# Kernel optimization log

Hardware: AMD Instinct MI355X
Metric: run time of the kernel (lower is better)

## Reference

```python
import jax, jax.numpy as jnp
import numpy as np

B, R, L, D, V, P = 128, 30, 60, 300, 50000, 3

def setup_inputs() -> dict:
    key = jax.random.key(0)
    ks = jax.random.split(key, 24)
    u = lambda k, shp: jax.random.uniform(k, shp, jnp.float32, -0.1, 0.1)
    inp = {
        'user_reviews': jax.random.randint(ks[0], (B, R, L), 0, V),
        'item_reviews': jax.random.randint(ks[1], (B, R, L), 0, V),
        'user_emb': u(ks[2], (V, D)),
        'item_emb': u(ks[3], (V, D)),
        'g1_w': u(ks[4], (D, D)), 'g1_b': u(ks[5], (D,)),
        'g2_w': u(ks[6], (D, D)), 'g2_b': u(ks[7], (D,)),
        # per-pointer review-level co-attention params (gumbel=True, pooling=max)
        'Mr': jax.random.normal(ks[8], (P, D, D)),
        'Wur': jax.random.normal(ks[9], (P, D, D)) * 0.05, 'bur': jnp.zeros((P, D)),
        'Wir': jax.random.normal(ks[10], (P, D, D)) * 0.05, 'bir': jnp.zeros((P, D)),
        # per-pointer word-level co-attention params (gumbel=False, pooling=avg)
        'Mw': jax.random.normal(ks[11], (P, D, D)),
        'Wuw': jax.random.normal(ks[12], (P, D, D)) * 0.05, 'buw': jnp.zeros((P, D)),
        'Wiw': jax.random.normal(ks[13], (P, D, D)) * 0.05, 'biw': jnp.zeros((P, D)),
        # FM params, pred_in_dim = 2*P*D (pointer_agg='concat')
        'fm_w0': jnp.zeros((1,)),
        'fm_w': jnp.zeros((2 * P * D,)),
        'fm_v': jax.random.normal(ks[14], (2 * P * D, 10)) * 0.01,
    }
    return inp

def _review_gate(embs, g1_w, g1_b, g2_w, g2_b):
    # embs: [B,R,L,D] -> [B,R,D]
    s = embs.sum(2)
    return jax.nn.sigmoid(s @ g1_w.T + g1_b) * jnp.tanh(s @ g2_w.T + g2_b)

def _coatt_scores(u_fea, i_fea, Wu, bu, Wi, bi, M):
    u = u_fea @ Wu.T + bu
    i = i_fea @ Wi.T + bi
    return jnp.einsum('brd,de,bse->brs', u, M, i)  # [B,R,R] or [B,L,L]

def reference(user_reviews, item_reviews, user_emb, item_emb,
              g1_w, g1_b, g2_w, g2_b,
              Mr, Wur, bur, Wir, bir,
              Mw, Wuw, buw, Wiw, biw,
              fm_w0, fm_w, fm_v):
    gkey = jax.random.key(42)
    u_embs = user_emb[user_reviews]  # [B,R,L,D]
    i_embs = item_emb[item_reviews]
    u_rev = _review_gate(u_embs, g1_w, g1_b, g2_w, g2_b)  # [B,R,D]
    i_rev = _review_gate(i_embs, g1_w, g1_b, g2_w, g2_b)
    u_reps, i_reps = [], []
    for p in range(P):
        # review-level co-attention, max pooling, gumbel hard (top-1 pointer)
        s = _coatt_scores(u_rev, i_rev, Wur[p], bur[p], Wir[p], bir[p], Mr[p])
        u_score = s.max(2)   # [B,R]
        i_score = s.max(1)   # [B,R]
        gu = jax.random.gumbel(jax.random.fold_in(gkey, 2 * p), u_score.shape)
        gi = jax.random.gumbel(jax.random.fold_in(gkey, 2 * p + 1), i_score.shape)
        # hard one-hot bmm gather + .long() re-embed == argmax review select
        # (the .long() cast in torch severs the straight-through grad path)
        idx_u = jnp.argmax(u_score + gu, axis=1)  # [B]
        idx_i = jnp.argmax(i_score + gi, axis=1)
        u_tok = jnp.take_along_axis(user_reviews, idx_u[:, None, None], axis=1)[:, 0]  # [B,L]
        i_tok = jnp.take_along_axis(item_reviews, idx_i[:, None, None], axis=1)[:, 0]
        u_words = user_emb[u_tok]  # [B,L,D]
        i_words = item_emb[i_tok]
        # word-level co-attention, avg pooling, soft attention
        s2 = _coatt_scores(u_words, i_words, Wuw[p], buw[p], Wiw[p], biw[p], Mw[p])
        p_u = jax.nn.softmax(s2.mean(2), axis=1)  # [B,L]
        p_i = jax.nn.softmax(s2.mean(1), axis=1)
        u_reps.append(jnp.einsum('bld,bl->bd', u_words, p_u))
        i_reps.append(jnp.einsum('bld,bl->bd', i_words, p_i))
    u_fea = jnp.concatenate(u_reps, axis=1)  # [B, P*D] (pointer_agg='concat')
    i_fea = jnp.concatenate(i_reps, axis=1)
    joint = jnp.concatenate([u_fea, i_fea], axis=1)  # [B, 2*P*D]; dropout is identity (eval)
    # Factorization Machine
    linear = fm_w0 + jnp.sum(fm_w * joint, axis=1, keepdims=True)
    inter = 0.5 * jnp.sum((joint @ fm_v) ** 2 - (joint ** 2) @ (fm_v ** 2), axis=1, keepdims=True)
    return (linear + inter)[:, 0]  # [B]
```

## Files before the change

kernel.cpp:

```cpp
#include <hip/hip_runtime.h>
#include <stdint.h>
#include <math.h>


__host__ __device__ static inline void tf2x32(uint32_t k0, uint32_t k1,
                                              uint32_t x0, uint32_t x1,
                                              uint32_t* o0, uint32_t* o1) {
  uint32_t ks[3] = {k0, k1, k0 ^ k1 ^ 0x1BD11BDAu};
  x0 += ks[0]; x1 += ks[1];
  const int rotA[4] = {13, 15, 26, 6};
  const int rotB[4] = {17, 29, 16, 24};
#pragma unroll
  for (int i = 0; i < 5; ++i) {
    const int* rot = ((i & 1) == 0) ? rotA : rotB;
#pragma unroll
    for (int j = 0; j < 4; ++j) {
      x0 += x1;
      x1 = (x1 << rot[j]) | (x1 >> (32 - rot[j]));
      x1 ^= x0;
    }
    x0 += ks[(i + 1) % 3];
    x1 += ks[(i + 2) % 3] + (uint32_t)(i + 1);
  }
  *o0 = x0; *o1 = x1;
}

struct GKeys { uint32_t v[12]; };
struct Ptr6 {
  const float* X[6];
  const float* W[6];
  const float* Bb[6];
  float*       Y[6];
};

__device__ static inline float jax_gumbel32(uint32_t k0, uint32_t k1, uint32_t idx) {
  uint32_t o0, o1;
  tf2x32(k0, k1, 0u, idx, &o0, &o1);
  uint32_t bits = o0 ^ o1;
  float f = __uint_as_float((bits >> 9) | 0x3f800000u) - 1.0f;
  float u = (f > 0.0f) ? f : 1.17549435e-38f;
  return -logf(-logf(u));
}

#define MODE_NN 0
#define MODE_NT 1
#define MODE_TN 2

template <int MODE, bool BIAS>
__device__ __forceinline__ void gemm_tile(float* __restrict__ sm,
                                          const float* __restrict__ X,
                                          const float* __restrict__ W,
                                          const float* __restrict__ bias,
                                          float* __restrict__ Y,
                                          float* __restrict__ Yt,
                                          int M, int bm, int n0, int t) {
  float (*Xs)[68] = (float(*)[68])sm;
  float (*Ws_)[68] = (float(*)[68])(sm + 20 * 68);
  const bool act = t < 256;
  int tm4 = ((t >> 4) & 15) * 4;
  int tn4 = (t & 15) * 4;
  float acc[4][4] = {{0.f}};
  int xm = t >> 2;
  int xk = (t & 3) * 5;
  for (int k0 = 0; k0 < 300; k0 += 20) {
    if (act) {
      if (MODE == MODE_TN) {
#pragma unroll
        for (int i = 0; i < 5; ++i) {
          int flat = t + i * 256;
          int kk = flat >> 6, nn = flat & 63;
          int r = bm + nn;
          Xs[kk][nn] = (r < 300) ? X[(size_t)(k0 + kk) * 300 + r] : 0.f;
        }
      } else {
        int rr = bm + xm; if (rr >= M) rr = M - 1;
        const float* xp = X + (size_t)rr * 300 + k0 + xk;
#pragma unroll
        for (int j = 0; j < 5; ++j) Xs[xk + j][xm] = xp[j];
      }
      if (MODE == MODE_NT) {
        int d = n0 + xm;
        bool ok = d < 300;
        const float* wp = W + (size_t)d * 300 + k0 + xk;
#pragma unroll
        for (int j = 0; j < 5; ++j) Ws_[xk + j][xm] = ok ? wp[j] : 0.f;
      } else {
#pragma unroll
        for (int i = 0; i < 5; ++i) {
          int flat = t + i * 256;
          int kk = flat >> 6, nn = flat & 63;
          int col = n0 + nn;
          Ws_[kk][nn] = (col < 300) ? W[(size_t)(k0 + kk) * 300 + col] : 0.f;
        }
      }
    }
    __syncthreads();
    if (act) {
#pragma unroll
      for (int kk = 0; kk < 20; ++kk) {
        const float4 a = *(const float4*)&Xs[kk][tm4];
        const float4 w = *(const float4*)&Ws_[kk][tn4];
        float av[4] = {a.x, a.y, a.z, a.w};
        float wv[4] = {w.x, w.y, w.z, w.w};
#pragma unroll
        for (int i = 0; i < 4; ++i)
#pragma unroll
          for (int j = 0; j < 4; ++j)
            acc[i][j] = fmaf(av[i], wv[j], acc[i][j]);
      }
    }
    __syncthreads();
  }
  if (!act) return;
  float bv[4] = {0.f, 0.f, 0.f, 0.f};
  if (BIAS) {
#pragma unroll
    for (int j = 0; j < 4; ++j) {
      int col = n0 + tn4 + j;
      if (col < 300) bv[j] = bias[col];
    }
  }
#pragma unroll
  for (int i = 0; i < 4; ++i) {
    int row = bm + tm4 + i;
    if (row < M) {
      float* yp = Y + (size_t)row * 300 + n0 + tn4;
#pragma unroll
      for (int j = 0; j < 4; ++j) {
        int col = n0 + tn4 + j;
        if (col < 300) yp[j] = acc[i][j] + bv[j];
      }
    }
  }
  if (Yt) {
#pragma unroll
    for (int i = 0; i < 4; ++i) {
      int row = bm + tm4 + i;
      if (row < 300) {
#pragma unroll
        for (int j = 0; j < 4; ++j) {
          int col = n0 + tn4 + j;
          if (col < 300) Yt[(size_t)col * 300 + row] = acc[i][j];
        }
      }
    }
  }
}

__global__ __launch_bounds__(256)
void weights_kernel(const float* __restrict__ Wur, const float* __restrict__ Mr,
                    const float* __restrict__ Mw, const float* __restrict__ Wiw,
                    const float* __restrict__ Wuw,
                    const float* __restrict__ bur, const float* __restrict__ buw,
                    const float* __restrict__ biw,
                    float* __restrict__ Wp, float* __restrict__ A1,
                    float* __restrict__ CGH, float* __restrict__ Bp) {
  __shared__ __align__(16) float arena[2720];
  int bid = blockIdx.x, t = threadIdx.x;
  if (bid < 75) {
    int z = bid / 25, r = bid % 25;
    gemm_tile<MODE_TN, false>(arena, Wur + (size_t)z * 90000, Mr + (size_t)z * 90000,
                              nullptr, Wp + (size_t)z * 90000, nullptr,
                              300, (r / 5) * 64, (r % 5) * 64, t);
  } else if (bid < 150) {
    int zi = bid - 75, z = zi / 25, r = zi % 25;
    gemm_tile<MODE_NN, false>(arena, Mw + (size_t)z * 90000, Wiw + (size_t)z * 90000,
                              nullptr, A1 + (size_t)z * 90000, nullptr,
                              300, (r / 5) * 64, (r % 5) * 64, t);
  } else {
    int z = bid - 150;
    float* vb = arena;
    float* t1s = arena + 304;
    float* t2s = arena + 608;
    const float* Mwz = Mw + (size_t)z * 90000;
    const float* Wuwz = Wuw + (size_t)z * 90000;
    const float* Wiwz = Wiw + (size_t)z * 90000;
    const float* Mrz = Mr + (size_t)z * 90000;
    for (int k = t; k < 300; k += 256) vb[k] = biw[z * 300 + k];
    __syncthreads();
    for (int e = t; e < 300; e += 256) {
      float a = 0.f;
      for (int k = 0; k < 300; ++k) a = fmaf(Mwz[(size_t)e * 300 + k], vb[k], a);
      t1s[e] = a;
    }
    __syncthreads();
    for (int k = t; k < 300; k += 256) {
      float a = 0.f;
      for (int d = 0; d < 300; ++d) a = fmaf(Wuwz[(size_t)d * 300 + k], t1s[d], a);
      CGH[(size_t)(2 * z) * 300 + k] = a;
    }
    __syncthreads();
    for (int d = t; d < 300; d += 256) vb[d] = buw[z * 300 + d];
    __syncthreads();
    for (int e = t; e < 300; e += 256) {
      float a = 0.f;
      for (int d = 0; d < 300; ++d) a = fmaf(Mwz[(size_t)d * 300 + e], vb[d], a);
      t2s[e] = a;
    }
    __syncthreads();
    for (int k = t; k < 300; k += 256) {
      float a = 0.f;
      for (int e = 0; e < 300; ++e) a = fmaf(Wiwz[(size_t)e * 300 + k], t2s[e], a);
      CGH[(size_t)(2 * z + 1) * 300 + k] = a;
    }
    __syncthreads();
    for (int d = t; d < 300; d += 256) vb[d] = bur[z * 300 + d];
    __syncthreads();
    for (int e = t; e < 300; e += 256) {
      float a = 0.f;
      for (int d = 0; d < 300; ++d) a = fmaf(Mrz[(size_t)d * 300 + e], vb[d], a);
      Bp[z * 300 + e] = a;
    }
  }
}

__global__ __launch_bounds__(320)
void gather_kernel(const int* __restrict__ uRevs, const int* __restrict__ iRevs,
                   const float* __restrict__ uEmb, const float* __restrict__ iEmb,
                   float* __restrict__ S) {
  int bid = blockIdx.x;
  int t = threadIdx.x;
  __shared__ int toks[4][60];
  if (t < 240) {
    int rr = t / 60, l = t - rr * 60;
    int grow = bid * 4 + rr;
    int side = grow / 3840;
    int row = grow - side * 3840;
    const int* revs = side ? iRevs : uRevs;
    toks[rr][l] = revs[row * 60 + l];
  }
  __syncthreads();
  if (t < 300) {
    int sub = t / 75;
    int q4 = (t - sub * 75) * 4;
    int grow = bid * 4 + sub;
    int side = grow / 3840;
    const float* emb = side ? iEmb : uEmb;
    const int* tk = toks[sub];
    float ax = 0.f, ay = 0.f, az = 0.f, aw = 0.f;
#pragma unroll
    for (int l0 = 0; l0 < 60; l0 += 15) {
      float4 v[15];
#pragma unroll
      for (int qq = 0; qq < 15; ++qq)
        v[qq] = *(const float4*)&emb[(size_t)tk[l0 + qq] * 300 + q4];
#pragma unroll
      for (int qq = 0; qq < 15; ++qq) {
        ax += v[qq].x; ay += v[qq].y; az += v[qq].z; aw += v[qq].w;
      }
    }
    float4 r = {ax, ay, az, aw};
    *(float4*)&S[(size_t)grow * 300 + q4] = r;
  }
}

__global__ __launch_bounds__(256)
void gate_kernel(const float* __restrict__ S,
                 const float* __restrict__ g1w, const float* __restrict__ g1b,
                 const float* __restrict__ g2w, const float* __restrict__ g2b,
                 float* __restrict__ REV,
                 const float* __restrict__ Wuw, const float* __restrict__ A1,
                 float* __restrict__ KG, float* __restrict__ KGT) {
  __shared__ __align__(16) float arena[4080];
  int bid = blockIdx.x, t = threadIdx.x;
  if (bid < 600) {
    float (*Xs)[68] = (float(*)[68])arena;
    float (*Ws1)[68] = (float(*)[68])(arena + 1360);
    float (*Ws2)[68] = (float(*)[68])(arena + 2720);
    int bm = (bid / 5) * 64;
    int n0 = (bid % 5) * 64;
    int tm4 = (t >> 4) * 4;
    int tn4 = (t & 15) * 4;
    float acc1[4][4] = {{0.f}};
    float acc2[4][4] = {{0.f}};
    int xm = t >> 2;
    int xk = (t & 3) * 5;
    for (int k0 = 0; k0 < 300; k0 += 20) {
      const float* xp = S + (size_t)(bm + xm) * 300 + k0 + xk;
#pragma unroll
      for (int j = 0; j < 5; ++j) Xs[xk + j][xm] = xp[j];
      {
        int dIdx = n0 + xm;
        bool ok = dIdx < 300;
        const float* wp1 = g1w + (size_t)dIdx * 300 + k0 + xk;
        const float* wp2 = g2w + (size_t)dIdx * 300 + k0 + xk;
#pragma unroll
        for (int j = 0; j < 5; ++j) Ws1[xk + j][xm] = ok ? wp1[j] : 0.f;
#pragma unroll
        for (int j = 0; j < 5; ++j) Ws2[xk + j][xm] = ok ? wp2[j] : 0.f;
      }
      __syncthreads();
#pragma unroll
      for (int kk = 0; kk < 20; ++kk) {
        const float4 a = *(const float4*)&Xs[kk][tm4];
        const float4 w1 = *(const float4*)&Ws1[kk][tn4];
        const float4 w2 = *(const float4*)&Ws2[kk][tn4];
        float av[4] = {a.x, a.y, a.z, a.w};
        float w1v[4] = {w1.x, w1.y, w1.z, w1.w};
        float w2v[4] = {w2.x, w2.y, w2.z, w2.w};
#pragma unroll
        for (int i = 0; i < 4; ++i)
#pragma unroll
          for (int j = 0; j < 4; ++j) {
            acc1[i][j] = fmaf(av[i], w1v[j], acc1[i][j]);
            acc2[i][j] = fmaf(av[i], w2v[j], acc2[i][j]);
          }
      }
      __syncthreads();
    }
#pragma unroll
    for (int i = 0; i < 4; ++i) {
      int row = bm + tm4 + i;
      float* yp = REV + (size_t)row * 300 + n0 + tn4;
#pragma unroll
      for (int j = 0; j < 4; ++j) {
        int col = n0 + tn4 + j;
        if (col < 300) {
          float a = acc1[i][j] + g1b[col];
          float b = acc2[i][j] + g2b[col];
          yp[j] = (1.f / (1.f + expf(-a))) * tanhf(b);
        }
      }
    }
  } else {
    int zi = bid - 600, z = zi / 25, r = zi % 25;
    gemm_tile<MODE_TN, false>(arena, Wuw + (size_t)z * 90000, A1 + (size_t)z * 90000,
                              nullptr, KG + (size_t)z * 90000,
                              KGT + (size_t)z * 90000,
                              300, (r / 5) * 64, (r % 5) * 64, t);
  }
}

__global__ __launch_bounds__(256)
void rev128_kernel(Ptr6 P) {
  int z = blockIdx.z;
  const bool nt = z >= 3;
  const float* __restrict__ X = P.X[z];
  const float* __restrict__ W = P.W[z];
  const float* __restrict__ bias = P.Bb[z];
  float* __restrict__ Y = P.Y[z];
  __shared__ __align__(16) float Xs[20][136];
  __shared__ __align__(16) float Ws_[20][68];
  int t = threadIdx.x;
  int bm = blockIdx.x * 128, n0 = blockIdx.y * 64;
  int tm8 = (t >> 4) * 8, tn4 = (t & 15) * 4;
  float acc[8][4] = {{0.f}};
  int xm = t >> 1, xk = (t & 1) * 10;
  int wm = t >> 2, wk = (t & 3) * 5;
  for (int k0 = 0; k0 < 300; k0 += 20) {
    const float* xp = X + (size_t)(bm + xm) * 300 + k0 + xk;
#pragma unroll
    for (int j = 0; j < 10; ++j) Xs[xk + j][xm] = xp[j];
    if (nt) {
      int d = n0 + wm;
      bool ok = d < 300;
      const float* wp = W + (size_t)d * 300 + k0 + wk;
#pragma unroll
      for (int j = 0; j < 5; ++j) Ws_[wk + j][wm] = ok ? wp[j] : 0.f;
    } else {
#pragma unroll
      for (int i = 0; i < 5; ++i) {
        int flat = t + i * 256;
        int kk = flat >> 6, nn = flat & 63;
        int col = n0 + nn;
        Ws_[kk][nn] = (col < 300) ? W[(size_t)(k0 + kk) * 300 + col] : 0.f;
      }
    }
    __syncthreads();
#pragma unroll
    for (int kk = 0; kk < 20; ++kk) {
      const float4 a0 = *(const float4*)&Xs[kk][tm8];
      const float4 a1 = *(const float4*)&Xs[kk][tm8 + 4];
      const float4 w = *(const float4*)&Ws_[kk][tn4];
      float av[8] = {a0.x, a0.y, a0.z, a0.w, a1.x, a1.y, a1.z, a1.w};
      float wv[4] = {w.x, w.y, w.z, w.w};
#pragma unroll
      for (int i = 0; i < 8; ++i)
#pragma unroll
        for (int j = 0; j < 4; ++j)
          acc[i][j] = fmaf(av[i], wv[j], acc[i][j]);
    }
    __syncthreads();
  }
  float bv[4];
#pragma unroll
  for (int j = 0; j < 4; ++j) {
    int col = n0 + tn4 + j;
    bv[j] = (col < 300) ? bias[col] : 0.f;
  }
#pragma unroll
  for (int i = 0; i < 8; ++i) {
    float* yp = Y + (size_t)(bm + tm8 + i) * 300 + n0 + tn4;
#pragma unroll
    for (int j = 0; j < 4; ++j) {
      int col = n0 + tn4 + j;
      if (col < 300) yp[j] = acc[i][j] + bv[j];
    }
  }
}

__global__ __launch_bounds__(256)
void argmax_mean_kernel(const float* __restrict__ Tall, const float* __restrict__ Iall,
                        const int* __restrict__ uRevs, const int* __restrict__ iRevs,
                        const float* __restrict__ uEmb, const float* __restrict__ iEmb,
                        int* __restrict__ idxU, int* __restrict__ idxI,
                        float* __restrict__ MEAN, GKeys K) {
  int b = blockIdx.x, z = blockIdx.y, t = threadIdx.x;
  uint32_t ku0 = K.v[z * 4], ku1 = K.v[z * 4 + 1];
  uint32_t ki0 = K.v[z * 4 + 2], ki1 = K.v[z * 4 + 3];
  __shared__ __align__(16) float Is[30 * 304];
  __shared__ float Sc[900];
  __shared__ float us[30], vs[30];
  __shared__ int selU, selI;
  __shared__ int toksI_s[60], toksU_s[60];
  const float* Tb = Tall + (size_t)z * 1152000 + (size_t)b * 9000;
  const float* Ib = Iall + (size_t)z * 1152000 + (size_t)b * 9000;
  for (int fc = t; fc < 2250; fc += 256) {
    int r = fc / 75, q = fc - r * 75;
    *(float4*)&Is[r * 304 + q * 4] = *(const float4*)&Ib[r * 300 + q * 4];
  }
  __syncthreads();
  for (int id = t; id < 900; id += 256) {
    int r = id / 30, c = id - r * 30;
    const float* tr = Tb + r * 300;
    const float* ic = Is + c * 304;
    float acc = 0.f;
    for (int k = 0; k < 300; k += 4) {
      float4 a = *(const float4*)&tr[k];
      float4 w = *(const float4*)&ic[k];
      acc = fmaf(a.x, w.x, acc);
      acc = fmaf(a.y, w.y, acc);
      acc = fmaf(a.z, w.z, acc);
      acc = fmaf(a.w, w.w, acc);
    }
    Sc[id] = acc;
  }
  __syncthreads();
  if (t < 30) {
    float m = -3.4e38f;
    for (int c = 0; c < 30; ++c) m = fmaxf(m, Sc[t * 30 + c]);
    us[t] = m + jax_gumbel32(ku0, ku1, (uint32_t)(b * 30 + t));
  } else if (t >= 64 && t < 94) {
    int s = t - 64;
    float m = -3.4e38f;
    for (int r = 0; r < 30; ++r) m = fmaxf(m, Sc[r * 30 + s]);
    vs[s] = m + jax_gumbel32(ki0, ki1, (uint32_t)(b * 30 + s));
  }
  __syncthreads();
  if (t == 0) {
    int best = 0; float bvv = us[0];
    for (int r = 1; r < 30; ++r) { if (us[r] > bvv) { bvv = us[r]; best = r; } }
    idxU[z * 128 + b] = best; selU = best;
  } else if (t == 1) {
    int best = 0; float bvv = vs[0];
    for (int s = 1; s < 30; ++s) { if (vs[s] > bvv) { bvv = vs[s]; best = s; } }
    idxI[z * 128 + b] = best; selI = best;
  }
  __syncthreads();
  if (t < 60) toksI_s[t] = iRevs[(b * 30 + selI) * 60 + t];
  else if (t >= 64 && t < 124) toksU_s[t - 64] = uRevs[(b * 30 + selU) * 60 + (t - 64)];
  __syncthreads();
  for (int dd = t; dd < 600; dd += 256) {
    int side = dd / 300;
    int d = dd - side * 300;
    const int* tk = side ? toksU_s : toksI_s;
    const float* em = side ? uEmb : iEmb;
    float acc = 0.f;
#pragma unroll
    for (int l0 = 0; l0 < 60; l0 += 10) {
      float v[10];
#pragma unroll
      for (int q = 0; q < 10; ++q)
        v[q] = em[(size_t)tk[l0 + q] * 300 + d];
#pragma unroll
      for (int q = 0; q < 10; ++q) acc += v[q];
    }
    MEAN[((size_t)(2 * z + side) * 128 + b) * 300 + d] = acc * (1.f / 60.f);
  }
}

__global__ __launch_bounds__(256)
void word_rep_kernel(const int* __restrict__ uRevs, const int* __restrict__ iRevs,
                     const float* __restrict__ uEmb, const float* __restrict__ iEmb,
                     const int* __restrict__ idxU, const int* __restrict__ idxI,
                     const float* __restrict__ MEAN, const float* __restrict__ KG,
                     const float* __restrict__ KGT, const float* __restrict__ CGH,
                     float* __restrict__ JNT) {
  int b = blockIdx.x, side = blockIdx.y, p = blockIdx.z;
  int zz = 2 * p + side;
  const int* revs = side ? iRevs : uRevs;
  const float* emb = side ? iEmb : uEmb;
  int idx = side ? idxI[p * 128 + b] : idxU[p * 128 + b];
  const float* Kmat = (side ? KGT : KG) + (size_t)p * 90000;
  __shared__ int toks[60];
  __shared__ float ms[300];
  __shared__ float g_s[300];
  __shared__ float score[60];
  __shared__ float probs[64];
  int t = threadIdx.x;
  if (t < 60) toks[t] = revs[(b * 30 + idx) * 60 + t];
  const float* mrow = MEAN + ((size_t)zz * 128 + b) * 300;
  for (int d = t; d < 300; d += 256) ms[d] = mrow[d];
  __syncthreads();
  for (int k = t; k < 300; k += 256) {
    const float* kr = Kmat + (size_t)k * 300;
    float acc = 0.f;
    for (int e = 0; e < 300; e += 4) {
      float4 kv = *(const float4*)&kr[e];
      acc = fmaf(kv.x, ms[e], acc);
      acc = fmaf(kv.y, ms[e + 1], acc);
      acc = fmaf(kv.z, ms[e + 2], acc);
      acc = fmaf(kv.w, ms[e + 3], acc);
    }
    g_s[k] = acc + CGH[(size_t)zz * 300 + k];
  }
  __syncthreads();
  int w = t >> 6, j = t & 63;
  for (int i = 0; i < 15; ++i) {
    int l = w * 15 + i;
    const float* er = emb + (size_t)toks[l] * 300;
    float partial = 0.f;
#pragma unroll
    for (int c = 0; c < 5; ++c) {
      int k = j + c * 64;
      if (k < 300) partial = fmaf(er[k], g_s[k], partial);
    }
#pragma unroll
    for (int m = 32; m >= 1; m >>= 1) partial += __shfl_xor(partial, m);
    if (j == 0) score[l] = partial;
  }
  __syncthreads();
  if (w == 0) {
    float s = (j < 60) ? score[j] : -3.4e38f;
    float m = s;
#pragma unroll
    for (int mm = 32; mm >= 1; mm >>= 1) m = fmaxf(m, __shfl_xor(m, mm));
    float e = (j < 60) ? expf(s - m) : 0.f;
    float sum = e;
#pragma unroll
    for (int mm = 32; mm >= 1; mm >>= 1) sum += __shfl_xor(sum, mm);
    if (j < 60) probs[j] = e / sum;
  }
  __syncthreads();
  float* outp = JNT + (size_t)b * 1800 + side * 900 + p * 300;
  for (int d = t; d < 300; d += 256) {
    float acc = 0.f;
    for (int l0 = 0; l0 < 60; l0 += 6) {
      float e0 = emb[(size_t)toks[l0 + 0] * 300 + d];
      float e1 = emb[(size_t)toks[l0 + 1] * 300 + d];
      float e2 = emb[(size_t)toks[l0 + 2] * 300 + d];
      float e3 = emb[(size_t)toks[l0 + 3] * 300 + d];
      float e4 = emb[(size_t)toks[l0 + 4] * 300 + d];
      float e5 = emb[(size_t)toks[l0 + 5] * 300 + d];
      acc = fmaf(probs[l0 + 0], e0, acc);
      acc = fmaf(probs[l0 + 1], e1, acc);
      acc = fmaf(probs[l0 + 2], e2, acc);
      acc = fmaf(probs[l0 + 3], e3, acc);
      acc = fmaf(probs[l0 + 4], e4, acc);
      acc = fmaf(probs[l0 + 5], e5, acc);
    }
    outp[d] = acc;
  }
}

__global__ __launch_bounds__(64)
void fm_kernel(const float* __restrict__ JNT, const float* __restrict__ w0,
               const float* __restrict__ fw, const float* __restrict__ fv,
               float* __restrict__ out) {
  int b = blockIdx.x, lane = threadIdx.x;
  const float* x = JNT + (size_t)b * 1800;
  float lin = 0.f;
  float t1[10], t2[10];
#pragma unroll
  for (int k = 0; k < 10; ++k) { t1[k] = 0.f; t2[k] = 0.f; }
  for (int j = lane; j < 1800; j += 64) {
    float xv = x[j];
    lin = fmaf(fw[j], xv, lin);
    float xx = xv * xv;
#pragma unroll
    for (int k = 0; k < 10; ++k) {
      float v = fv[j * 10 + k];
      t1[k] = fmaf(xv, v, t1[k]);
      t2[k] = fmaf(xx, v * v, t2[k]);
    }
  }
#pragma unroll
  for (int m = 32; m >= 1; m >>= 1) {
    lin += __shfl_xor(lin, m);
#pragma unroll
    for (int k = 0; k < 10; ++k) {
      t1[k] += __shfl_xor(t1[k], m);
      t2[k] += __shfl_xor(t2[k], m);
    }
  }
  if (lane == 0) {
    float inter = 0.f;
#pragma unroll
    for (int k = 0; k < 10; ++k) inter += t1[k] * t1[k] - t2[k];
    out[b] = w0[0] + lin + 0.5f * inter;
  }
}

extern "C" void kernel_launch(void* const* d_in, const int* in_sizes, int n_in,
                              void* d_out, int out_size, void* d_ws, size_t ws_size,
                              hipStream_t stream) {
  (void)in_sizes; (void)n_in; (void)out_size;
  const int*   uRevs = (const int*)d_in[0];
  const int*   iRevs = (const int*)d_in[1];
  const float* uEmb  = (const float*)d_in[2];
  const float* iEmb  = (const float*)d_in[3];
  const float* g1w   = (const float*)d_in[4];
  const float* g1b   = (const float*)d_in[5];
  const float* g2w   = (const float*)d_in[6];
  const float* g2b   = (const float*)d_in[7];
  const float* Mr    = (const float*)d_in[8];
  const float* Wur   = (const float*)d_in[9];
  const float* bur   = (const float*)d_in[10];
  const float* Wir   = (const float*)d_in[11];
  const float* bir   = (const float*)d_in[12];
  const float* Mw    = (const float*)d_in[13];
  const float* Wuw   = (const float*)d_in[14];
  const float* buw   = (const float*)d_in[15];
  const float* Wiw   = (const float*)d_in[16];
  const float* biw   = (const float*)d_in[17];
  const float* fmw0  = (const float*)d_in[18];
  const float* fmw   = (const float*)d_in[19];
  const float* fmv   = (const float*)d_in[20];
  float* out = (float*)d_out;

  float* ws = (float*)d_ws;
  const size_t NEED_BYTES = (size_t)10298700 * 4;
  if (ws_size < NEED_BYTES) return;

  float* S     = ws + 0;
  float* TPall = ws + 0;
  float* REV   = ws + 3456000;
  float* MEAN  = ws + 3456000;
  float* JNT   = ws + 3916800;
  int*   idxU  = (int*)(ws + 4147200);
  int*   idxI  = idxU + 384;
  float* IPall = ws + 5760000;
  float* A1    = ws + 9216000;
  float* Wp    = ws + 9486000;
  float* KG    = ws + 9756000;
  float* KGT   = ws + 10026000;
  float* Bp    = ws + 10296000;
  float* CGH   = ws + 10296900;

  weights_kernel<<<dim3(153), dim3(256), 0, stream>>>(
      Wur, Mr, Mw, Wiw, Wuw, bur, buw, biw, Wp, A1, CGH, Bp);

  gather_kernel<<<dim3(1920), dim3(320), 0, stream>>>(
      uRevs, iRevs, uEmb, iEmb, S);

  gate_kernel<<<dim3(675), dim3(256), 0, stream>>>(
      S, g1w, g1b, g2w, g2b, REV, Wuw, A1, KG, KGT);

  {
    Ptr6 P;
    for (int z = 0; z < 3; ++z) {
      P.X[z] = REV;
      P.W[z] = Wp + (size_t)z * 90000;
      P.Bb[z] = Bp + z * 300;
      P.Y[z] = TPall + (size_t)z * 1152000;
      P.X[z + 3] = REV + (size_t)3840 * 300;
      P.W[z + 3] = Wir + (size_t)z * 90000;
      P.Bb[z + 3] = bir + z * 300;
      P.Y[z + 3] = IPall + (size_t)z * 1152000;
    }
    rev128_kernel<<<dim3(30, 5, 6), dim3(256), 0, stream>>>(P);
  }

  {
    GKeys K;
    for (int p = 0; p < 3; ++p) {
      tf2x32(0u, 42u, 0u, (uint32_t)(2 * p),     &K.v[p * 4],     &K.v[p * 4 + 1]);
      tf2x32(0u, 42u, 0u, (uint32_t)(2 * p + 1), &K.v[p * 4 + 2], &K.v[p * 4 + 3]);
    }
    argmax_mean_kernel<<<dim3(128, 3), dim3(256), 0, stream>>>(
        TPall, IPall, uRevs, iRevs, uEmb, iEmb, idxU, idxI, MEAN, K);
  }

  word_rep_kernel<<<dim3(128, 2, 3), dim3(256), 0, stream>>>(
      uRevs, iRevs, uEmb, iEmb, idxU, idxI, MEAN, KG, KGT, CGH, JNT);

  fm_kernel<<<dim3(128), dim3(64), 0, stream>>>(JNT, fmw0, fmw, fmv, out);
}
```

Measured before the change: 392.7 us.

## Fold weight-precompute kernel into gate and rev128 launches to cut a launch

Removes the standalone weights kernel. Its GEMM tiles and bias-vector work now run as extra blocks in gate_kernel, and the KG/KGT GEMM moves into rev128_kernel as extra blocks, which works because A1 is then ready. This drops one kernel launch and lets the small weight GEMMs overlap with the gate and projection work. The first matrix-vector product in the bias path is also changed to a wave-parallel shuffle reduction, and rev128 now uses a flattened 1D grid with a shared arena.

```diff
diff --git a/kernel.cpp b/kernel.cpp
--- a/kernel.cpp
+++ b/kernel.cpp
@@ -147,73 +147,6 @@
   }
 }
 
-__global__ __launch_bounds__(256)
-void weights_kernel(const float* __restrict__ Wur, const float* __restrict__ Mr,
-                    const float* __restrict__ Mw, const float* __restrict__ Wiw,
-                    const float* __restrict__ Wuw,
-                    const float* __restrict__ bur, const float* __restrict__ buw,
-                    const float* __restrict__ biw,
-                    float* __restrict__ Wp, float* __restrict__ A1,
-                    float* __restrict__ CGH, float* __restrict__ Bp) {
-  __shared__ __align__(16) float arena[2720];
-  int bid = blockIdx.x, t = threadIdx.x;
-  if (bid < 75) {
-    int z = bid / 25, r = bid % 25;
-    gemm_tile<MODE_TN, false>(arena, Wur + (size_t)z * 90000, Mr + (size_t)z * 90000,
-                              nullptr, Wp + (size_t)z * 90000, nullptr,
-                              300, (r / 5) * 64, (r % 5) * 64, t);
-  } else if (bid < 150) {
-    int zi = bid - 75, z = zi / 25, r = zi % 25;
-    gemm_tile<MODE_NN, false>(arena, Mw + (size_t)z * 90000, Wiw + (size_t)z * 90000,
-                              nullptr, A1 + (size_t)z * 90000, nullptr,
-                              300, (r / 5) * 64, (r % 5) * 64, t);
-  } else {
-    int z = bid - 150;
-    float* vb = arena;
-    float* t1s = arena + 304;
-    float* t2s = arena + 608;
-    const float* Mwz = Mw + (size_t)z * 90000;
-    const float* Wuwz = Wuw + (size_t)z * 90000;
-    const float* Wiwz = Wiw + (size_t)z * 90000;
-    const float* Mrz = Mr + (size_t)z * 90000;
-    for (int k = t; k < 300; k += 256) vb[k] = biw[z * 300 + k];
-    __syncthreads();
-    for (int e = t; e < 300; e += 256) {
-      float a = 0.f;
-      for (int k = 0; k < 300; ++k) a = fmaf(Mwz[(size_t)e * 300 + k], vb[k], a);
-      t1s[e] = a;
-    }
-    __syncthreads();
-    for (int k = t; k < 300; k += 256) {
-      float a = 0.f;
-      for (int d = 0; d < 300; ++d) a = fmaf(Wuwz[(size_t)d * 300 + k], t1s[d], a);
-      CGH[(size_t)(2 * z) * 300 + k] = a;
-    }
-    __syncthreads();
-    for (int d = t; d < 300; d += 256) vb[d] = buw[z * 300 + d];
-    __syncthreads();
-    for (int e = t; e < 300; e += 256) {
-      float a = 0.f;
-      for (int d = 0; d < 300; ++d) a = fmaf(Mwz[(size_t)d * 300 + e], vb[d], a);
-      t2s[e] = a;
-    }
-    __syncthreads();
-    for (int k = t; k < 300; k += 256) {
-      float a = 0.f;
-      for (int e = 0; e < 300; ++e) a = fmaf(Wiwz[(size_t)e * 300 + k], t2s[e], a);
-      CGH[(size_t)(2 * z + 1) * 300 + k] = a;
-    }
-    __syncthreads();
-    for (int d = t; d < 300; d += 256) vb[d] = bur[z * 300 + d];
-    __syncthreads();
-    for (int e = t; e < 300; e += 256) {
-      float a = 0.f;
-      for (int d = 0; d < 300; ++d) a = fmaf(Mrz[(size_t)d * 300 + e], vb[d], a);
-      Bp[z * 300 + e] = a;
-    }
-  }
-}
-
 __global__ __launch_bounds__(320)
 void gather_kernel(const int* __restrict__ uRevs, const int* __restrict__ iRevs,
                    const float* __restrict__ uEmb, const float* __restrict__ iEmb,
@@ -259,8 +192,13 @@
                  const float* __restrict__ g1w, const float* __restrict__ g1b,
                  const float* __restrict__ g2w, const float* __restrict__ g2b,
                  float* __restrict__ REV,
-                 const float* __restrict__ Wuw, const float* __restrict__ A1,
-                 float* __restrict__ KG, float* __restrict__ KGT) {
+                 const float* __restrict__ Wur, const float* __restrict__ Mr,
+                 const float* __restrict__ Mw, const float* __restrict__ Wiw,
+                 const float* __restrict__ Wuw,
+                 const float* __restrict__ bur, const float* __restrict__ buw,
+                 const float* __restrict__ biw,
+                 float* __restrict__ Wp, float* __restrict__ A1,
+                 float* __restrict__ CGH, float* __restrict__ Bp) {
   __shared__ __align__(16) float arena[4080];
   int bid = blockIdx.x, t = threadIdx.x;
   if (bid < 600) {
@@ -322,27 +260,98 @@
         }
       }
     }
+  } else if (bid < 675) {
+    int zi = bid - 600, z = zi / 25, r = zi % 25;
+    gemm_tile<MODE_TN, false>(arena, Wur + (size_t)z * 90000, Mr + (size_t)z * 90000,
+                              nullptr, Wp + (size_t)z * 90000, nullptr,
+                              300, (r / 5) * 64, (r % 5) * 64, t);
+  } else if (bid < 750) {
+    int zi = bid - 675, z = zi / 25, r = zi % 25;
+    gemm_tile<MODE_NN, false>(arena, Mw + (size_t)z * 90000, Wiw + (size_t)z * 90000,
+                              nullptr, A1 + (size_t)z * 90000, nullptr,
+                              300, (r / 5) * 64, (r % 5) * 64, t);
   } else {
-    int zi = bid - 600, z = zi / 25, r = zi % 25;
+    int z = bid - 750;
+    float* vb = arena;
+    float* t1s = arena + 304;
+    float* t2s = arena + 608;
+    const float* Mwz = Mw + (size_t)z * 90000;
+    const float* Wuwz = Wuw + (size_t)z * 90000;
+    const float* Wiwz = Wiw + (size_t)z * 90000;
+    const float* Mrz = Mr + (size_t)z * 90000;
+    for (int k = t; k < 300; k += 256) vb[k] = biw[z * 300 + k];
+    __syncthreads();
+    {
+      int w = t >> 6, j = t & 63;
+      for (int i = 0; i < 75; ++i) {
+        int e = w * 75 + i;
+        float partial = 0.f;
+#pragma unroll
+        for (int c = 0; c < 5; ++c) {
+          int k = j + c * 64;
+          if (k < 300) partial = fmaf(Mwz[(size_t)e * 300 + k], vb[k], partial);
+        }
+#pragma unroll
+        for (int m = 32; m >= 1; m >>= 1) partial += __shfl_xor(partial, m);
+        if (j == 0) t1s[e] = partial;
+      }
+    }
+    __syncthreads();
+    for (int k = t; k < 300; k += 256) {
+      float a = 0.f;
+      for (int d = 0; d < 300; ++d) a = fmaf(Wuwz[(size_t)d * 300 + k], t1s[d], a);
+      CGH[(size_t)(2 * z) * 300 + k] = a;
+    }
+    __syncthreads();
+    for (int d = t; d < 300; d += 256) vb[d] = buw[z * 300 + d];
+    __syncthreads();
+    for (int e = t; e < 300; e += 256) {
+      float a = 0.f;
+      for (int d = 0; d < 300; ++d) a = fmaf(Mwz[(size_t)d * 300 + e], vb[d], a);
+      t2s[e] = a;
+    }
+    __syncthreads();
+    for (int k = t; k < 300; k += 256) {
+      float a = 0.f;
+      for (int e = 0; e < 300; ++e) a = fmaf(Wiwz[(size_t)e * 300 + k], t2s[e], a);
+      CGH[(size_t)(2 * z + 1) * 300 + k] = a;
+    }
+    __syncthreads();
+    for (int d = t; d < 300; d += 256) vb[d] = bur[z * 300 + d];
+    __syncthreads();
+    for (int e = t; e < 300; e += 256) {
+      float a = 0.f;
+      for (int d = 0; d < 300; ++d) a = fmaf(Mrz[(size_t)d * 300 + e], vb[d], a);
+      Bp[z * 300 + e] = a;
+    }
+  }
+}
+
+__global__ __launch_bounds__(256)
+void rev128_kernel(Ptr6 P, const float* __restrict__ Wuw,
+                   const float* __restrict__ A1,
+                   float* __restrict__ KG, float* __restrict__ KGT) {
+  __shared__ __align__(16) float arena[4080];
+  int bid = blockIdx.x, t = threadIdx.x;
+  if (bid >= 900) {
+    int zi = bid - 900, z = zi / 25, r = zi % 25;
     gemm_tile<MODE_TN, false>(arena, Wuw + (size_t)z * 90000, A1 + (size_t)z * 90000,
                               nullptr, KG + (size_t)z * 90000,
                               KGT + (size_t)z * 90000,
                               300, (r / 5) * 64, (r % 5) * 64, t);
-  }
-}
-
-__global__ __launch_bounds__(256)
-void rev128_kernel(Ptr6 P) {
-  int z = blockIdx.z;
+    return;
+  }
+  int z = bid / 150;
+  int rem = bid - z * 150;
+  int bm = (rem % 30) * 128;
+  int n0 = (rem / 30) * 64;
   const bool nt = z >= 3;
   const float* __restrict__ X = P.X[z];
   const float* __restrict__ W = P.W[z];
   const float* __restrict__ bias = P.Bb[z];
   float* __restrict__ Y = P.Y[z];
-  __shared__ __align__(16) float Xs[20][136];
-  __shared__ __align__(16) float Ws_[20][68];
-  int t = threadIdx.x;
-  int bm = blockIdx.x * 128, n0 = blockIdx.y * 64;
+  float (*Xs)[136] = (float(*)[136])arena;
+  float (*Ws_)[68] = (float(*)[68])(arena + 2720);
   int tm8 = (t >> 4) * 8, tn4 = (t & 15) * 4;
   float acc[8][4] = {{0.f}};
   int xm = t >> 1, xk = (t & 1) * 10;
@@ -647,14 +656,12 @@
   float* Bp    = ws + 10296000;
   float* CGH   = ws + 10296900;
 
-  weights_kernel<<<dim3(153), dim3(256), 0, stream>>>(
-      Wur, Mr, Mw, Wiw, Wuw, bur, buw, biw, Wp, A1, CGH, Bp);
-
   gather_kernel<<<dim3(1920), dim3(320), 0, stream>>>(
       uRevs, iRevs, uEmb, iEmb, S);
 
-  gate_kernel<<<dim3(675), dim3(256), 0, stream>>>(
-      S, g1w, g1b, g2w, g2b, REV, Wuw, A1, KG, KGT);
+  gate_kernel<<<dim3(753), dim3(256), 0, stream>>>(
+      S, g1w, g1b, g2w, g2b, REV,
+      Wur, Mr, Mw, Wiw, Wuw, bur, buw, biw, Wp, A1, CGH, Bp);
 
   {
     Ptr6 P;
@@ -668,7 +675,7 @@
       P.Bb[z + 3] = bir + z * 300;
       P.Y[z + 3] = IPall + (size_t)z * 1152000;
     }
-    rev128_kernel<<<dim3(30, 5, 6), dim3(256), 0, stream>>>(P);
+    rev128_kernel<<<dim3(975), dim3(256), 0, stream>>>(P, Wuw, A1, KG, KGT);
   }
 
   {
```

New measurement: 402.8 us. 2.6% more time.
